# Performance work log

Measured on AMD Instinct MI355X. Metric: run time of the kernel, lower is better.

The kernel has to match this reference:

```python
import jax, jax.numpy as jnp
import numpy as np
import hashlib

VOCAB_SIZE = 50257
EMBED_DIM = 1024
NUM_BUCKETS = 10000
BATCH, SEQ = 8, 4096


def _md5_bucket(token_id: int) -> int:
    # Exactly the module's hash_token: md5 of the decimal string, mod num_buckets.
    return int(hashlib.md5(str(token_id).encode()).hexdigest(), 16) % NUM_BUCKETS


def setup_inputs() -> dict:
    key = jax.random.key(0)
    k_ids, k_emb = jax.random.split(key)
    input_ids = jax.random.randint(k_ids, (BATCH, SEQ), 0, VOCAB_SIZE, dtype=jnp.int64)
    # Deterministic integer hash of input_ids (host-side, matches torch .item() loop).
    ids_np = np.asarray(input_ids)
    # Hash only the unique tokens, then map back -- same result, far fewer md5 calls.
    uniq, inv = np.unique(ids_np, return_inverse=True)
    bucket_of_uniq = np.array([_md5_bucket(int(t)) for t in uniq], dtype=np.int64)
    hashed_ids = jnp.asarray(bucket_of_uniq[inv].reshape(ids_np.shape))
    # nn.Embedding default init: N(0, 1)
    embedding = jax.random.normal(k_emb, (NUM_BUCKETS, EMBED_DIM), dtype=jnp.float32)
    return {"input_ids": input_ids, "hashed_ids": hashed_ids, "embedding": embedding}


def reference(input_ids, hashed_ids, embedding):
    # hashed_ids = md5(input_ids) % num_buckets (precomputed constant int map);
    # forward is an embedding gather reshaped to [*input_ids.shape, embed_dim].
    flat = hashed_ids.reshape(-1)                 # [B*S]
    out = jnp.take(embedding, flat, axis=0)       # [B*S, D]
    return out.reshape(*input_ids.shape, embedding.shape[-1])  # [B, S, D]
```

## Files before the change

### kernel.cpp

```cpp
#include <hip/hip_runtime.h>


#define ROW_VEC     256
#define NUM_BUCKETS 10000

__global__ __launch_bounds__(256) void HashEmbedding_46136538693901_kernel(
    const int* __restrict__ hashed_ids,
    const uint4* __restrict__ emb,
    uint4* __restrict__ out,
    int n_vec)
{
    int i = blockIdx.x * blockDim.x + threadIdx.x;
    if (i >= n_vec) return;
    int row = i >> 8;
    int col = i & (ROW_VEC - 1);
    int idx = hashed_ids[row];
    if ((unsigned)idx >= (unsigned)NUM_BUCKETS) idx = 0;
    out[i] = emb[(size_t)idx * ROW_VEC + col];
}

extern "C" void kernel_launch(void* const* d_in, const int* in_sizes, int n_in,
                              void* d_out, int out_size, void* d_ws, size_t ws_size,
                              hipStream_t stream) {
    const int*   hashed = (const int*)d_in[1];
    const uint4* emb    = (const uint4*)d_in[2];
    uint4*       out    = (uint4*)d_out;

    int n_tokens = in_sizes[1];
    int n_vec    = n_tokens * ROW_VEC;

    int block = 256;
    int grid  = (n_vec + block - 1) / block;
    HashEmbedding_46136538693901_kernel<<<grid, block, 0, stream>>>(hashed, emb, out, n_vec);
}
```

Before: 179.6 us.

## Gather eight tokens per block with batched loads and nontemporal stores

Each block now handles eight token rows: it loads all eight bucket indices, issues eight independent 16-byte loads per thread, then writes the results with nontemporal stores. This is meant to raise memory-level parallelism per thread, cut the per-element index loads, and keep streaming output writes from evicting the embedding table from cache. Running fewer blocks reduces scheduling overhead but keeps more registers live per thread.

```diff
diff --git a/kernel.cpp b/kernel.cpp
--- a/kernel.cpp
+++ b/kernel.cpp
@@ -1,35 +1,53 @@
 #include <hip/hip_runtime.h>
 
 
-#define ROW_VEC     256
-#define NUM_BUCKETS 10000
+#define ROW_VEC       256
+#define NUM_BUCKETS   10000
+#define TOK_PER_BLOCK 8
+
+typedef unsigned int u32x4 __attribute__((ext_vector_type(4)));
 
 __global__ __launch_bounds__(256) void HashEmbedding_46136538693901_kernel(
     const int* __restrict__ hashed_ids,
-    const uint4* __restrict__ emb,
-    uint4* __restrict__ out,
-    int n_vec)
+    const u32x4* __restrict__ emb,
+    u32x4* __restrict__ out,
+    int n_tokens)
 {
-    int i = blockIdx.x * blockDim.x + threadIdx.x;
-    if (i >= n_vec) return;
-    int row = i >> 8;
-    int col = i & (ROW_VEC - 1);
-    int idx = hashed_ids[row];
-    if ((unsigned)idx >= (unsigned)NUM_BUCKETS) idx = 0;
-    out[i] = emb[(size_t)idx * ROW_VEC + col];
+    const int t0  = blockIdx.x * TOK_PER_BLOCK;
+    const int col = threadIdx.x;
+
+    int idx[TOK_PER_BLOCK];
+#pragma unroll
+    for (int t = 0; t < TOK_PER_BLOCK; ++t) {
+        int r = t0 + t;
+        idx[t] = (r < n_tokens) ? hashed_ids[r] : 0;
+        if ((unsigned)idx[t] >= (unsigned)NUM_BUCKETS) idx[t] = 0;
+    }
+
+    u32x4 v[TOK_PER_BLOCK];
+#pragma unroll
+    for (int t = 0; t < TOK_PER_BLOCK; ++t) {
+        v[t] = emb[(unsigned)(idx[t] * ROW_VEC + col)];
+    }
+
+#pragma unroll
+    for (int t = 0; t < TOK_PER_BLOCK; ++t) {
+        int r = t0 + t;
+        if (r < n_tokens) {
+            __builtin_nontemporal_store(v[t], &out[(size_t)r * ROW_VEC + col]);
+        }
+    }
 }
 
 extern "C" void kernel_launch(void* const* d_in, const int* in_sizes, int n_in,
                               void* d_out, int out_size, void* d_ws, size_t ws_size,
                               hipStream_t stream) {
     const int*   hashed = (const int*)d_in[1];
-    const uint4* emb    = (const uint4*)d_in[2];
-    uint4*       out    = (uint4*)d_out;
+    const u32x4* emb    = (const u32x4*)d_in[2];
+    u32x4*       outp   = (u32x4*)d_out;
 
     int n_tokens = in_sizes[1];
-    int n_vec    = n_tokens * ROW_VEC;
-
-    int block = 256;
-    int grid  = (n_vec + block - 1) / block;
-    HashEmbedding_46136538693901_kernel<<<grid, block, 0, stream>>>(hashed, emb, out, n_vec);
+    int grid = (n_tokens + TOK_PER_BLOCK - 1) / TOK_PER_BLOCK;
+    HashEmbedding_46136538693901_kernel<<<grid, 256, 0, stream>>>(
+        hashed, emb, outp, n_tokens);
 }
```

After: 179.8 us. Within noise of the previous version (+0.1%).
